# Kernel optimization log

Measured on AMD Instinct MI355X. Metric: run time of the kernel, lower is better.

## Reference

```python
import jax, jax.numpy as jnp
import numpy as np

B, CIN, X, Y = 4, 3, 128, 128
D, L, DEPTH, OUT = 64, 8, 4, 1
GRID_RANGE = 1.0
LN_EPS = 1e-5
YR = Y // 2 + 1


def _build_phi_f():
    # 1D Hilbert-matrix eigenbases along each axis, outer product, then rfft2.
    def top_eigvecs(n):
        i = np.arange(n)
        Z = 1.0 / (i[:, None] + i[None, :] + 1.0)  # Hilbert matrix, float64
        w, V = np.linalg.eigh(Z)
        idx = np.argsort(-w)[:L]
        return V.T[idx]  # (L, n)

    Vx = top_eigvecs(X)
    Vy = top_eigvecs(Y)
    phi = Vx[:, :, None] * Vy[:, None, :]  # (L, X, Y) separable eigenfunctions
    Phi_f = np.fft.rfft2(phi, s=(X, Y))  # (L, X, YR)
    return jnp.asarray(Phi_f, dtype=jnp.complex64)


def setup_inputs() -> dict:
    key = jax.random.key(0)
    ks = jax.random.split(key, 16)
    u = lambda k, shape, bound: jax.random.uniform(k, shape, jnp.float32, -bound, bound)
    inv = 1.0 / np.sqrt(D)
    inp = {
        "x": jax.random.normal(ks[0], (B, CIN, X, Y), jnp.float32),
        "Phi_f": _build_phi_f(),  # constant buffer
        "lift_w": u(ks[1], (D, CIN + 2), 1.0 / np.sqrt(CIN + 2)),
        "lift_b": u(ks[2], (D,), 1.0 / np.sqrt(CIN + 2)),
        "Theta": u(ks[3], (DEPTH, L, D, D), 1.0 / D),  # kaiming_uniform(a=sqrt(5)) ~ U(-1/d, 1/d)
        "glu_val_w": u(ks[4], (DEPTH, D, D), inv),
        "glu_val_b": u(ks[5], (DEPTH, D), inv),
        "glu_gate_w": u(ks[6], (DEPTH, D, D), inv),
        "glu_gate_b": u(ks[7], (DEPTH, D), inv),
        "ln_g": jnp.ones((DEPTH, D), jnp.float32),
        "ln_b": jnp.zeros((DEPTH, D), jnp.float32),
        "head_w": u(ks[8], (OUT, D), inv),
        "head_b": u(ks[9], (OUT,), inv),
    }
    return inp


def _stu_layer(h, Phi_f, Theta, vw, vb, gw, gb, g, b):
    # LayerNorm over channel dim (torch LayerNorm on channels-last view)
    ht = jnp.transpose(h, (0, 2, 3, 1))  # (B, X, Y, D)
    mu = jnp.mean(ht, axis=-1, keepdims=True)
    var = jnp.var(ht, axis=-1, keepdims=True)
    zt = (ht - mu) * jax.lax.rsqrt(var + LN_EPS) * g + b
    z = jnp.transpose(zt, (0, 3, 1, 2))  # (B, D, X, Y)

    Xf = jnp.fft.rfftn(z, axes=(-2, -1))  # (B, D, X, YR) complex
    Uf = Xf[:, :, None, :, :] * jnp.conj(Phi_f)[None, None]  # (B, D, L, X, YR)
    U = jnp.fft.irfftn(Uf, s=(X, Y), axes=(-2, -1))  # (B, D, L, X, Y)
    # einsum('bdlxy,lhd->bhlxy') followed by sum over l, fused:
    S = jnp.einsum("bdlxy,lhd->bhxy", U, Theta)

    V = jnp.einsum("bhxy,oh->boxy", S, vw) + vb[None, :, None, None]
    G = jax.nn.sigmoid(jnp.einsum("bhxy,oh->boxy", S, gw) + gb[None, :, None, None])
    return h + V * G


def reference(x, Phi_f, lift_w, lift_b, Theta, glu_val_w, glu_val_b,
              glu_gate_w, glu_gate_b, ln_g, ln_b, head_w, head_b):
    bsz = x.shape[0]
    # add_2d_grid: append yy, xx coordinate channels
    ys = jnp.linspace(0.0, GRID_RANGE, X, dtype=x.dtype)
    xs = jnp.linspace(0.0, GRID_RANGE, Y, dtype=x.dtype)
    yy, xx = jnp.meshgrid(ys, xs, indexing="ij")
    yy = jnp.broadcast_to(yy[None, None], (bsz, 1, X, Y))
    xx = jnp.broadcast_to(xx[None, None], (bsz, 1, X, Y))
    h = jnp.concatenate([x, yy, xx], axis=1)  # (B, CIN+2, X, Y)

    # LocalLift2D with kernel_size=1 -> pointwise conv
    h = jnp.einsum("bcxy,dc->bdxy", h, lift_w) + lift_b[None, :, None, None]

    for i in range(DEPTH):
        h = _stu_layer(h, Phi_f, Theta[i], glu_val_w[i], glu_val_b[i],
                       glu_gate_w[i], glu_gate_b[i], ln_g[i], ln_b[i])

    y = jnp.einsum("bdxy,od->boxy", h, head_w) + head_b[None, :, None, None]
    return y
```

## Files before the change

kernel.cpp:

```cpp
#include <hip/hip_runtime.h>
#include <math.h>
#include <string.h>


#define NXY 16384

#define OFF_V       16
#define OFF_MC      1040
#define OFF_THETAA  132112
#define OFF_AG      263184
#define OFF_Z       295952
#define OFF_S       2393104
#define OFF_H       4490256
#define OFF_P       8684560
#define WS_NEED_F   25461776ULL

typedef short short8 __attribute__((ext_vector_type(8)));
typedef float float4m __attribute__((ext_vector_type(4)));

__device__ __forceinline__ unsigned short bf_rn(float f) {
    unsigned u = __float_as_uint(f);
    u += 0x7fffu + ((u >> 16) & 1u);
    return (unsigned short)(u >> 16);
}
__device__ __forceinline__ float bf_tof(unsigned short s) {
    return __uint_as_float(((unsigned)s) << 16);
}

__global__ void poison_out(float* out) { out[0] = 1e9f; }


static float vhost[1024];

static void host_hilbert_topk(float* outv) {
    static double Vs[8][128];
    static double W[8][128];
    double recip[256];
    for (int i = 0; i < 256; i++) recip[i] = 1.0 / (double)(i + 1);
    for (int j = 0; j < 8; j++)
        for (int i = 0; i < 128; i++) Vs[j][i] = recip[i + j];
    for (int outer = 0; outer < 25; outer++) {
        for (int half = 0; half < 2; half++) {
            for (int j = 0; j < 8; j++)
                for (int i = 0; i < 128; i++) {
                    double s = 0.0;
                    for (int k = 0; k < 128; k++) s += Vs[j][k] * recip[i + k];
                    W[j][i] = s;
                }
            memcpy(Vs, W, sizeof(Vs));
        }
        for (int j = 0; j < 8; j++) {
            for (int p = 0; p < j; p++) {
                double d = 0.0;
                for (int i = 0; i < 128; i++) d += Vs[j][i] * Vs[p][i];
                for (int i = 0; i < 128; i++) Vs[j][i] -= d * Vs[p][i];
            }
            double nn = 0.0;
            for (int i = 0; i < 128; i++) nn += Vs[j][i] * Vs[j][i];
            double inv = 1.0 / sqrt(nn);
            for (int i = 0; i < 128; i++) Vs[j][i] *= inv;
        }
    }
    for (int j = 0; j < 8; j++)
        for (int i = 0; i < 128; i++) outv[j * 128 + i] = (float)Vs[j][i];
}

namespace {
struct VInit {
    VInit() { host_hilbert_topk(vhost); }
};
VInit vinit_once;
}

__global__ void build_mct(const float* __restrict__ v, unsigned short* __restrict__ McT) {
    int l = blockIdx.y;
    int idx = blockIdx.x * 256 + threadIdx.x;
    int r = idx >> 7, k = idx & 127;
    McT[l * 16384 + idx] = bf_rn(v[l * 128 + ((k - r) & 127)]);
}


__global__ void build_thetaAHL(const float* __restrict__ Theta, unsigned short* __restrict__ ThA) {
    int i = blockIdx.x * 256 + threadIdx.x;
    int k = i & 127; int r = i >> 7;
    int m = r & 127; r >>= 7;
    int tile = r & 3; int dep = r >> 2;
    int l2 = m >> 6, hch = m & 63, d = k & 63;
    float f = Theta[(((dep * 8 + tile * 2 + l2) * 64) + hch) * 64 + d];
    unsigned short hb = bf_rn(f);
    ThA[i] = (k < 64) ? hb : bf_rn(f - bf_tof(hb));
}

__global__ void build_AG(const float* __restrict__ vw, const float* __restrict__ gw,
                         float* __restrict__ AG) {
    int i = blockIdx.x * 256 + threadIdx.x;
    int m = i & 127; int r = i >> 7; int h = r & 63; int dep = r >> 6;
    int o = m >> 1;
    const float* W = (m & 1) ? gw : vw;
    AG[i] = W[(dep * 64 + o) * 64 + h];
}


__global__ void lift_ln(const float* __restrict__ x, const float* __restrict__ lw,
                        const float* __restrict__ lb, const float* __restrict__ g0,
                        const float* __restrict__ b0, float* __restrict__ h,
                        unsigned short* __restrict__ zT) {
    __shared__ float w[320];
    __shared__ float bsm[64];
    __shared__ float gs[64], bs[64];
    int tid = threadIdx.x;
    for (int i = tid; i < 320; i += 256) w[i] = lw[i];
    if (tid < 64) { bsm[tid] = lb[tid]; gs[tid] = g0[tid]; bs[tid] = b0[tid]; }
    __syncthreads();
    int b = blockIdx.y;
    int xy = blockIdx.x * 256 + tid;
    int xi = xy >> 7, yi = xy & 127;
    float c0 = x[(size_t)(b * 3 + 0) * NXY + xy];
    float c1 = x[(size_t)(b * 3 + 1) * NXY + xy];
    float c2 = x[(size_t)(b * 3 + 2) * NXY + xy];
    float yyv = xi * (1.0f / 127.0f), xxv = yi * (1.0f / 127.0f);
    float vv[64];
    float sum = 0.f;
#pragma unroll
    for (int d = 0; d < 64; d++) {
        float acc = bsm[d] + w[d * 5] * c0 + w[d * 5 + 1] * c1 + w[d * 5 + 2] * c2
                  + w[d * 5 + 3] * yyv + w[d * 5 + 4] * xxv;
        vv[d] = acc;
        sum += acc;
        h[(size_t)(b * 64 + d) * NXY + xy] = acc;
    }
    float mu = sum * (1.0f / 64.0f);
    float vs = 0.f;
#pragma unroll
    for (int d = 0; d < 64; d++) { float t = vv[d] - mu; vs += t * t; }
    float inv = rsqrtf(vs * (1.0f / 64.0f) + 1e-5f);
    unsigned short t16[64];
#pragma unroll
    for (int d = 0; d < 64; d++) t16[d] = bf_rn((vv[d] - mu) * inv * gs[d] + bs[d]);
    unsigned short* zp = zT + ((size_t)b * NXY + xy) * 64;
#pragma unroll
    for (int i = 0; i < 8; i++) {
        uint4 pk;
        pk.x = (unsigned)t16[8 * i + 0] | ((unsigned)t16[8 * i + 1] << 16);
        pk.y = (unsigned)t16[8 * i + 2] | ((unsigned)t16[8 * i + 3] << 16);
        pk.z = (unsigned)t16[8 * i + 4] | ((unsigned)t16[8 * i + 5] << 16);
        pk.w = (unsigned)t16[8 * i + 6] | ((unsigned)t16[8 * i + 7] << 16);
        *(uint4*)(zp + 8 * i) = pk;
    }
}

__device__ __forceinline__ int sw_idx(int row, int k) {
    return row * 128 + ((((k >> 3) ^ (row & 7)) << 3) | (k & 7));
}
__device__ __forceinline__ int sw64(int row, int k) {
    return row * 64 + (((((k >> 3) ^ (row & 7)) & 7) << 3) | (k & 7));
}


__launch_bounds__(256)
__global__ void k1_mfma(const unsigned short* __restrict__ zT,
                        const unsigned short* __restrict__ ThA,
                        unsigned short* __restrict__ P) {
    __shared__ unsigned short st[16384];
    const int lhtile = blockIdx.x, x = blockIdx.y, b = blockIdx.z;
    const int tid = threadIdx.x;
    const int wid = tid >> 6, lane = tid & 63;
    const int ln15 = lane & 15, q = lane >> 4;
    const int ko = q * 8;
    const unsigned short* Ab = ThA + lhtile * 16384;
    const unsigned short* Bb = zT + ((size_t)b * NXY + x * 128) * 64;

    float4m acc[2][8];
#pragma unroll
    for (int mt = 0; mt < 2; mt++)
#pragma unroll
        for (int nt = 0; nt < 8; nt++) acc[mt][nt] = (float4m){0.f, 0.f, 0.f, 0.f};

#pragma unroll
    for (int k0 = 0; k0 < 128; k0 += 32) {
        short8 a[2];
#pragma unroll
        for (int mt = 0; mt < 2; mt++)
            a[mt] = *(const short8*)(Ab + (wid * 32 + mt * 16 + ln15) * 128 + k0 + ko);
        int d0 = (k0 & 63) + ko;
#pragma unroll
        for (int nt = 0; nt < 8; nt++) {
            int n = nt * 16 + ln15;
            short8 bf = *(const short8*)(Bb + n * 64 + d0);
#pragma unroll
            for (int mt = 0; mt < 2; mt++)
                acc[mt][nt] = __builtin_amdgcn_mfma_f32_16x16x32_bf16(a[mt], bf, acc[mt][nt], 0, 0, 0);
        }
    }
#pragma unroll
    for (int mt = 0; mt < 2; mt++)
#pragma unroll
        for (int nt = 0; nt < 8; nt++) {
            int y = nt * 16 + ln15;
            int r0 = wid * 32 + mt * 16 + q * 4;
            float av[4] = {acc[mt][nt].x, acc[mt][nt].y, acc[mt][nt].z, acc[mt][nt].w};
#pragma unroll
            for (int r = 0; r < 4; r++) st[sw_idx(r0 + r, y)] = bf_rn(av[r]);
        }
    __syncthreads();
    unsigned short* Pb = P + (size_t)(b * 512 + lhtile * 128) * NXY + x * 128;
#pragma unroll
    for (int i = 0; i < 8; i++) {
        int idx = i * 256 + tid;
        int m = idx >> 4, c = idx & 15;
        *(uint4*)(Pb + (size_t)m * NXY + c * 8) = *(const uint4*)&st[sw_idx(m, c * 8)];
    }
}


__launch_bounds__(256)
__global__ void corrsum_ys(const unsigned short* __restrict__ P,
                           const unsigned short* __restrict__ McT,
                           unsigned short* __restrict__ S) {
    __shared__ unsigned short Tt[8192];
    const int hh = blockIdx.x, yh = blockIdx.y, b = blockIdx.z;
    const int tid = threadIdx.x;
    const int wid = tid >> 6, lane = tid & 63;
    const int ln15 = lane & 15, q = lane >> 4;
    const int ko = q * 8;
    const int mrow0 = wid * 32 + ln15;
    const int yb = yh * 64;

    float4m accS[2][4];
#pragma unroll
    for (int mt = 0; mt < 2; mt++)
#pragma unroll
        for (int nt = 0; nt < 4; nt++) accS[mt][nt] = (float4m){0.f, 0.f, 0.f, 0.f};

    short8 apre[2][4][2];

    {
        const unsigned short* pl = P + ((size_t)(b * 8 + 0) * 64 + hh) * NXY;
#pragma unroll
        for (int k4 = 0; k4 < 4; k4++)
#pragma unroll
            for (int mt = 0; mt < 2; mt++)
                apre[0][k4][mt] = *(const short8*)(pl + (mrow0 + mt * 16) * 128 + k4 * 32 + ko);
    }

#pragma unroll
    for (int l = 0; l < 8; l++) {
        const unsigned short* Mc = McT + l * 16384;
        const int cb = l & 1, nb = cb ^ 1;

        float4m acc1[2][4];
#pragma unroll
        for (int mt = 0; mt < 2; mt++)
#pragma unroll
            for (int nt = 0; nt < 4; nt++) acc1[mt][nt] = (float4m){0.f, 0.f, 0.f, 0.f};
#pragma unroll
        for (int k4 = 0; k4 < 4; k4++) {
            int k0 = k4 * 32;
#pragma unroll
            for (int nt = 0; nt < 4; nt++) {
                int n = yb + nt * 16 + ln15;
                short8 bf = *(const short8*)(Mc + n * 128 + k0 + ko);
#pragma unroll
                for (int mt = 0; mt < 2; mt++)
                    acc1[mt][nt] = __builtin_amdgcn_mfma_f32_16x16x32_bf16(apre[cb][k4][mt], bf, acc1[mt][nt], 0, 0, 0);
            }
        }
#pragma unroll
        for (int mt = 0; mt < 2; mt++)
#pragma unroll
            for (int nt = 0; nt < 4; nt++) {
                int yo = nt * 16 + ln15;
                int x0 = wid * 32 + mt * 16 + q * 4;
                float av[4] = {acc1[mt][nt].x, acc1[mt][nt].y, acc1[mt][nt].z, acc1[mt][nt].w};
                unsigned short hs[4];
#pragma unroll
                for (int r = 0; r < 4; r++) hs[r] = bf_rn(av[r]);
                uint2 pk;
                pk.x = (unsigned)hs[0] | ((unsigned)hs[1] << 16);
                pk.y = (unsigned)hs[2] | ((unsigned)hs[3] << 16);
                *(uint2*)&Tt[sw_idx(yo, x0)] = pk;
            }
        __syncthreads();

        if (l < 7) {
            const unsigned short* pln = P + ((size_t)(b * 8 + l + 1) * 64 + hh) * NXY;
#pragma unroll
            for (int k4 = 0; k4 < 4; k4++)
#pragma unroll
                for (int mt = 0; mt < 2; mt++)
                    apre[nb][k4][mt] = *(const short8*)(pln + (mrow0 + mt * 16) * 128 + k4 * 32 + ko);
        }

#pragma unroll
        for (int k4 = 0; k4 < 4; k4++) {
            int k0 = k4 * 32;
            short8 a2[2];
#pragma unroll
            for (int mt = 0; mt < 2; mt++)
                a2[mt] = *(const short8*)(Mc + (mrow0 + mt * 16) * 128 + k0 + ko);
#pragma unroll
            for (int nt = 0; nt < 4; nt++) {
                int n = nt * 16 + ln15;
                short8 bf = *(const short8*)&Tt[sw_idx(n, k0 + ko)];
#pragma unroll
                for (int mt = 0; mt < 2; mt++)
                    accS[mt][nt] = __builtin_amdgcn_mfma_f32_16x16x32_bf16(a2[mt], bf, accS[mt][nt], 0, 0, 0);
            }
        }
        __syncthreads();
    }

#pragma unroll
    for (int mt = 0; mt < 2; mt++)
#pragma unroll
        for (int nt = 0; nt < 4; nt++) {
            int yl = nt * 16 + ln15;
            int x0 = wid * 32 + mt * 16 + q * 4;
            float av[4] = {accS[mt][nt].x, accS[mt][nt].y, accS[mt][nt].z, accS[mt][nt].w};
#pragma unroll
            for (int r = 0; r < 4; r++) Tt[sw64(x0 + r, yl)] = bf_rn(av[r]);
        }
    __syncthreads();
    unsigned short* Sb = S + ((size_t)(b * 64) + hh) * NXY + yb;
#pragma unroll
    for (int i = 0; i < 4; i++) {
        int idx = i * 256 + tid;
        int xr = idx >> 3, c = idx & 7;
        *(uint4*)(Sb + xr * 128 + c * 8) = *(const uint4*)&Tt[sw64(xr, c * 8)];
    }
}


template <int KTOT, long long BS1, long long PSTR, int NPART>
__launch_bounds__(256)
__global__ void glu_ln(const float* __restrict__ A0,
                       const unsigned short* __restrict__ B0, long long bsx, long long bsz,
                       float* __restrict__ C0, long long csx, long long csz, long long csm,
                       const float* __restrict__ e_vb, const float* __restrict__ e_gb,
                       const float* __restrict__ lngn, const float* __restrict__ lnbn,
                       unsigned short* __restrict__ zT,
                       const float* __restrict__ hw, const float* __restrict__ hbp,
                       float* __restrict__ outp) {
    constexpr int KS = 16;
    __shared__ float As[KS][132];
    __shared__ float Bs[KS][132];
    __shared__ float hn[64][129];
    const int tid = threadIdx.x;
    const int tm = tid >> 4, tn = tid & 15;
    const int m0 = tm * 8, n0 = tn * 8;
    const float* Ab = A0;
    const unsigned short* Bb = B0 + (long long)blockIdx.x * bsx + (long long)blockIdx.z * bsz;
    float* Cb = C0 + (long long)blockIdx.x * csx + (long long)blockIdx.z * csz;

    float acc[8][8];
#pragma unroll
    for (int i = 0; i < 8; i++)
#pragma unroll
        for (int j = 0; j < 8; j++) acc[i][j] = 0.f;

    for (int k0 = 0; k0 < KTOT; k0 += KS) {
#pragma unroll
        for (int i = 0; i < 2; i++) {
            int idx = tid + i * 256;
            int k = idx >> 5, f4 = (idx & 31) * 4;
            float4 v = *(const float4*)(Ab + (long long)(k0 + k) * 128 + f4);
            *(float4*)&As[k][f4] = v;
        }
#pragma unroll
        for (int i = 0; i < 2; i++) {
            int idx = tid + i * 256;
            int k = idx >> 5, f4 = (idx & 31) * 4;
            const unsigned short* bp = Bb + (long long)(k0 + k) * BS1 + f4;
            float vx = 0.f, vy = 0.f, vz = 0.f, vw = 0.f;
#pragma unroll
            for (int p = 0; p < NPART; p++) {
                uint2 t = *(const uint2*)(bp + (long long)p * PSTR);
                vx += bf_tof((unsigned short)(t.x & 0xffff));
                vy += bf_tof((unsigned short)(t.x >> 16));
                vz += bf_tof((unsigned short)(t.y & 0xffff));
                vw += bf_tof((unsigned short)(t.y >> 16));
            }
            Bs[k][f4] = vx; Bs[k][f4 + 1] = vy; Bs[k][f4 + 2] = vz; Bs[k][f4 + 3] = vw;
        }
        __syncthreads();
#pragma unroll
        for (int kk = 0; kk < KS; kk++) {
            float4 a0 = *(const float4*)&As[kk][m0];
            float4 a1 = *(const float4*)&As[kk][m0 + 4];
            float4 b0 = *(const float4*)&Bs[kk][n0];
            float4 b1 = *(const float4*)&Bs[kk][n0 + 4];
            float av[8] = {a0.x, a0.y, a0.z, a0.w, a1.x, a1.y, a1.z, a1.w};
            float bv[8] = {b0.x, b0.y, b0.z, b0.w, b1.x, b1.y, b1.z, b1.w};
#pragma unroll
            for (int i = 0; i < 8; i++)
#pragma unroll
                for (int j = 0; j < 8; j++) acc[i][j] += av[i] * bv[j];
        }
        __syncthreads();
    }

#pragma unroll
    for (int i = 0; i < 4; i++) {
        int o = (m0 >> 1) + i;
        float vbv = e_vb[o], gbv = e_gb[o];
        float* hp = Cb + (long long)o * csm + n0;
        float4 h0 = *(float4*)hp;
        float4 h1 = *(float4*)(hp + 4);
        float hv[8] = {h0.x, h0.y, h0.z, h0.w, h1.x, h1.y, h1.z, h1.w};
#pragma unroll
        for (int j = 0; j < 8; j++) {
            float V = acc[2 * i][j] + vbv;
            float G = acc[2 * i + 1][j] + gbv;
            float s = 1.0f / (1.0f + expf(-G));
            hv[j] += V * s;
            hn[o][n0 + j] = hv[j];
        }
        if (outp == nullptr) {
            float4 o0 = {hv[0], hv[1], hv[2], hv[3]};
            float4 o1 = {hv[4], hv[5], hv[6], hv[7]};
            *(float4*)hp = o0;
            *(float4*)(hp + 4) = o1;
        }
    }

    if (lngn != nullptr) {
        __syncthreads();
        if (tid < 128) {
            int xy = tid;
            float sum = 0.f;
#pragma unroll
            for (int d = 0; d < 64; d++) sum += hn[d][xy];
            float mu = sum * (1.0f / 64.0f);
            float vs = 0.f;
#pragma unroll
            for (int d = 0; d < 64; d++) { float t = hn[d][xy] - mu; vs += t * t; }
            float inv = rsqrtf(vs * (1.0f / 64.0f) + 1e-5f);
            unsigned short t16[64];
#pragma unroll
            for (int d = 0; d < 64; d++)
                t16[d] = bf_rn((hn[d][xy] - mu) * inv * lngn[d] + lnbn[d]);
            unsigned short* zp = zT + ((size_t)blockIdx.z * NXY + blockIdx.x * 128 + xy) * 64;
#pragma unroll
            for (int i = 0; i < 8; i++) {
                uint4 pk;
                pk.x = (unsigned)t16[8 * i + 0] | ((unsigned)t16[8 * i + 1] << 16);
                pk.y = (unsigned)t16[8 * i + 2] | ((unsigned)t16[8 * i + 3] << 16);
                pk.z = (unsigned)t16[8 * i + 4] | ((unsigned)t16[8 * i + 5] << 16);
                pk.w = (unsigned)t16[8 * i + 6] | ((unsigned)t16[8 * i + 7] << 16);
                *(uint4*)(zp + 8 * i) = pk;
            }
        }
    } else if (outp != nullptr) {
        __syncthreads();
        if (tid < 128) {
            int xy = tid;
            float acch = hbp[0];
#pragma unroll
            for (int d = 0; d < 64; d++) acch += hn[d][xy] * hw[d];
            outp[(size_t)blockIdx.z * NXY + blockIdx.x * 128 + xy] = acch;
        }
    }
}


extern "C" void kernel_launch(void* const* d_in, const int* in_sizes, int n_in,
                              void* d_out, int out_size, void* d_ws, size_t ws_size,
                              hipStream_t stream) {
    const float* x      = (const float*)d_in[0];
    const float* lift_w = (const float*)d_in[2];
    const float* lift_b = (const float*)d_in[3];
    const float* Theta  = (const float*)d_in[4];
    const float* vw     = (const float*)d_in[5];
    const float* vb     = (const float*)d_in[6];
    const float* gw     = (const float*)d_in[7];
    const float* gb     = (const float*)d_in[8];
    const float* ln_g   = (const float*)d_in[9];
    const float* ln_b   = (const float*)d_in[10];
    const float* head_w = (const float*)d_in[11];
    const float* head_b = (const float*)d_in[12];
    float* out = (float*)d_out;
    float* ws = (float*)d_ws;
    (void)in_sizes; (void)n_in; (void)out_size;

    float* v      = ws + OFF_V;
    unsigned short* McT = (unsigned short*)(ws + OFF_MC);
    unsigned short* ThA = (unsigned short*)(ws + OFF_THETAA);
    float* AG     = ws + OFF_AG;
    unsigned short* zT = (unsigned short*)(ws + OFF_Z);
    unsigned short* S  = (unsigned short*)(ws + OFF_S);
    float* h      = ws + OFF_H;
    unsigned short* P = (unsigned short*)(ws + OFF_P);

    hipMemcpyAsync(v, vhost, sizeof(vhost), hipMemcpyHostToDevice, stream);

    build_mct<<<dim3(64, 8), 256, 0, stream>>>(v, McT);
    build_thetaAHL<<<1024, 256, 0, stream>>>(Theta, ThA);
    build_AG<<<128, 256, 0, stream>>>(vw, gw, AG);

    lift_ln<<<dim3(64, 4), 256, 0, stream>>>(x, lift_w, lift_b, ln_g, ln_b, h, zT);

    for (int dep = 0; dep < 4; dep++) {
        k1_mfma<<<dim3(4, 128, 4), 256, 0, stream>>>(zT, ThA + dep * 65536, P);

        corrsum_ys<<<dim3(64, 2, 4), 256, 0, stream>>>(P, McT, S);

        const float* lngn = (dep < 3) ? (ln_g + (dep + 1) * 64) : nullptr;
        const float* lnbn = (dep < 3) ? (ln_b + (dep + 1) * 64) : nullptr;
        float* outp = (dep == 3) ? out : nullptr;
        glu_ln<64, 16384LL, 0LL, 1><<<dim3(128, 1, 4), 256, 0, stream>>>(
            AG + dep * 8192,
            S, 128, 1048576,
            h, 128, 1048576, 16384,
            vb + dep * 64, gb + dep * 64,
            lngn, lnbn, zT,
            head_w, head_b, outp);
    }

    if (ws_size < WS_NEED_F * 4ULL) {
        poison_out<<<1, 1, 0, stream>>>(out);
    }
}
```

Measured before the change: 556.0 us.

## Split corrsum L-loop across two wave groups and pin host constant buffer

The corrsum kernel now runs 512 threads per block. Two groups of four waves each handle half of the 8 eigen-modes with separate shared-memory staging buffers, and their fp32 partial sums are reduced through LDS before the bf16 store. The goal is more waves per block to hide latency on a grid of only 512 blocks, at the cost of doubled LDS use, an extra reduction step and higher register pressure. Separately, the host vector used in the per-call async memcpy is page-locked once via hipHostRegister, so the upload does not go through a pageable-staging copy.

New measurement: 578.2 us. +4.0%, slower.

```diff
diff --git a/kernel.cpp b/kernel.cpp
--- a/kernel.cpp
+++ b/kernel.cpp
@@ -213,17 +213,18 @@
 }
 
 
-__launch_bounds__(256)
-__global__ void corrsum_ys(const unsigned short* __restrict__ P,
+__launch_bounds__(512)
+__global__ void corrsum_ls(const unsigned short* __restrict__ P,
                            const unsigned short* __restrict__ McT,
                            unsigned short* __restrict__ S) {
-    __shared__ unsigned short Tt[8192];
+    __shared__ __align__(16) unsigned short Tt[2][8192];
     const int hh = blockIdx.x, yh = blockIdx.y, b = blockIdx.z;
     const int tid = threadIdx.x;
     const int wid = tid >> 6, lane = tid & 63;
+    const int lg = wid >> 2, wq = wid & 3;
     const int ln15 = lane & 15, q = lane >> 4;
     const int ko = q * 8;
-    const int mrow0 = wid * 32 + ln15;
+    const int mrow0 = wq * 32 + ln15;
     const int yb = yh * 64;
 
     float4m accS[2][4];
@@ -235,7 +236,7 @@
     short8 apre[2][4][2];
 
     {
-        const unsigned short* pl = P + ((size_t)(b * 8 + 0) * 64 + hh) * NXY;
+        const unsigned short* pl = P + ((size_t)(b * 8 + lg * 4) * 64 + hh) * NXY;
 #pragma unroll
         for (int k4 = 0; k4 < 4; k4++)
 #pragma unroll
@@ -244,9 +245,10 @@
     }
 
 #pragma unroll
-    for (int l = 0; l < 8; l++) {
+    for (int it = 0; it < 4; it++) {
+        const int l = lg * 4 + it;
         const unsigned short* Mc = McT + l * 16384;
-        const int cb = l & 1, nb = cb ^ 1;
+        const int cb = it & 1, nb = cb ^ 1;
 
         float4m acc1[2][4];
 #pragma unroll
@@ -270,7 +272,7 @@
 #pragma unroll
             for (int nt = 0; nt < 4; nt++) {
                 int yo = nt * 16 + ln15;
-                int x0 = wid * 32 + mt * 16 + q * 4;
+                int x0 = wq * 32 + mt * 16 + q * 4;
                 float av[4] = {acc1[mt][nt].x, acc1[mt][nt].y, acc1[mt][nt].z, acc1[mt][nt].w};
                 unsigned short hs[4];
 #pragma unroll
@@ -278,12 +280,12 @@
                 uint2 pk;
                 pk.x = (unsigned)hs[0] | ((unsigned)hs[1] << 16);
                 pk.y = (unsigned)hs[2] | ((unsigned)hs[3] << 16);
-                *(uint2*)&Tt[sw_idx(yo, x0)] = pk;
+                *(uint2*)&Tt[lg][sw_idx(yo, x0)] = pk;
             }
         __syncthreads();
 
-        if (l < 7) {
-            const unsigned short* pln = P + ((size_t)(b * 8 + l + 1) * 64 + hh) * NXY;
+        if (it < 3) {
+            const unsigned short* pln = P + ((size_t)(b * 8 + lg * 4 + it + 1) * 64 + hh) * NXY;
 #pragma unroll
             for (int k4 = 0; k4 < 4; k4++)
 #pragma unroll
@@ -301,7 +303,7 @@
 #pragma unroll
             for (int nt = 0; nt < 4; nt++) {
                 int n = nt * 16 + ln15;
-                short8 bf = *(const short8*)&Tt[sw_idx(n, k0 + ko)];
+                short8 bf = *(const short8*)&Tt[lg][sw_idx(n, k0 + ko)];
 #pragma unroll
                 for (int mt = 0; mt < 2; mt++)
                     accS[mt][nt] = __builtin_amdgcn_mfma_f32_16x16x32_bf16(a2[mt], bf, accS[mt][nt], 0, 0, 0);
@@ -310,23 +312,45 @@
         __syncthreads();
     }
 
-#pragma unroll
-    for (int mt = 0; mt < 2; mt++)
-#pragma unroll
-        for (int nt = 0; nt < 4; nt++) {
-            int yl = nt * 16 + ln15;
-            int x0 = wid * 32 + mt * 16 + q * 4;
-            float av[4] = {accS[mt][nt].x, accS[mt][nt].y, accS[mt][nt].z, accS[mt][nt].w};
-#pragma unroll
-            for (int r = 0; r < 4; r++) Tt[sw64(x0 + r, yl)] = bf_rn(av[r]);
-        }
+    float* fst = (float*)&Tt[0][0];
+    const int fbase = (wq * 64 + lane) * 32;
+    if (lg == 1) {
+#pragma unroll
+        for (int mt = 0; mt < 2; mt++)
+#pragma unroll
+            for (int nt = 0; nt < 4; nt++)
+                *(float4m*)&fst[fbase + (mt * 4 + nt) * 4] = accS[mt][nt];
+    }
+    __syncthreads();
+    if (lg == 0) {
+#pragma unroll
+        for (int mt = 0; mt < 2; mt++)
+#pragma unroll
+            for (int nt = 0; nt < 4; nt++)
+                accS[mt][nt] += *(const float4m*)&fst[fbase + (mt * 4 + nt) * 4];
+    }
+    __syncthreads();
+
+    unsigned short* Tf = &Tt[0][0];
+    if (lg == 0) {
+#pragma unroll
+        for (int mt = 0; mt < 2; mt++)
+#pragma unroll
+            for (int nt = 0; nt < 4; nt++) {
+                int yl = nt * 16 + ln15;
+                int x0 = wq * 32 + mt * 16 + q * 4;
+                float av[4] = {accS[mt][nt].x, accS[mt][nt].y, accS[mt][nt].z, accS[mt][nt].w};
+#pragma unroll
+                for (int r = 0; r < 4; r++) Tf[sw64(x0 + r, yl)] = bf_rn(av[r]);
+            }
+    }
     __syncthreads();
     unsigned short* Sb = S + ((size_t)(b * 64) + hh) * NXY + yb;
 #pragma unroll
-    for (int i = 0; i < 4; i++) {
-        int idx = i * 256 + tid;
+    for (int i = 0; i < 2; i++) {
+        int idx = i * 512 + tid;
         int xr = idx >> 3, c = idx & 7;
-        *(uint4*)(Sb + xr * 128 + c * 8) = *(const uint4*)&Tt[sw64(xr, c * 8)];
+        *(uint4*)(Sb + xr * 128 + c * 8) = *(const uint4*)&Tf[sw64(xr, c * 8)];
     }
 }
 
@@ -466,6 +490,12 @@
 extern "C" void kernel_launch(void* const* d_in, const int* in_sizes, int n_in,
                               void* d_out, int out_size, void* d_ws, size_t ws_size,
                               hipStream_t stream) {
+    static const bool v_pinned = []() {
+        hipError_t e = hipHostRegister(vhost, sizeof(vhost), hipHostRegisterDefault);
+        return e == hipSuccess;
+    }();
+    (void)v_pinned;
+
     const float* x      = (const float*)d_in[0];
     const float* lift_w = (const float*)d_in[2];
     const float* lift_b = (const float*)d_in[3];
@@ -502,7 +532,7 @@
     for (int dep = 0; dep < 4; dep++) {
         k1_mfma<<<dim3(4, 128, 4), 256, 0, stream>>>(zT, ThA + dep * 65536, P);
 
-        corrsum_ys<<<dim3(64, 2, 4), 256, 0, stream>>>(P, McT, S);
+        corrsum_ls<<<dim3(64, 2, 4), 512, 0, stream>>>(P, McT, S);
 
         const float* lngn = (dep < 3) ? (ln_g + (dep + 1) * 64) : nullptr;
         const float* lnbn = (dep < 3) ? (ln_b + (dep + 1) * 64) : nullptr;
```
